# Kernel tuning notes

Measured on AMD Instinct MI355X. Metric: run time of the kernel, lower is better.

Reference implementation:

```python
import jax, jax.numpy as jnp
import numpy as np

B, G, NB, NC = 1024, 28, 2, 20
THR_CONF = 3.0
THR_NMS = 0.3
K = 4096            # fixed top-k detection slots (jit-friendly padding)
NEG = jnp.float32(-1e30)


def setup_inputs() -> dict:
    key = jax.random.key(0)
    k1, k2, k3 = jax.random.split(key, 3)
    return {
        "p_boxes": jax.random.normal(k1, (B, G, G, NB * 4), dtype=jnp.float32),
        "p_confs": jax.random.normal(k2, (B, G, G, NB), dtype=jnp.float32),
        "p_clses": jax.random.normal(k3, (B, G, G, NC), dtype=jnp.float32),
    }


def _decode_topk(p_boxes, p_confs, p_clses):
    # boxes: (B,G,G,NB,4) with (offx, offy, w, h) per box slot
    boxes = p_boxes.reshape(B, G, G, NB, 4)
    col = jnp.arange(G, dtype=jnp.float32)
    row = jnp.arange(G, dtype=jnp.float32)
    # offxy2xy: xy = (offxy + colrow) / num_grid  (dim1=row, dim2=col per torch.where order)
    cx = (boxes[..., 0] + col[None, None, :, None]) / G
    cy = (boxes[..., 1] + row[None, :, None, None]) / G
    w, h = boxes[..., 2], boxes[..., 3]
    # xywh2ltrb
    ltrb = jnp.stack([cx - w * 0.5, cy - h * 0.5, cx + w * 0.5, cy + h * 0.5], axis=-1)
    # label = argmax over classes + 1, shared by both box slots of a cell
    labels = jnp.argmax(p_clses, axis=-1) + 1                       # (B,G,G)
    labels = jnp.broadcast_to(labels[..., None], (B, G, G, NB))
    bids = jnp.broadcast_to(jnp.arange(B)[:, None, None, None], (B, G, G, NB))
    valid = p_confs > THR_CONF

    N = B * G * G * NB
    scores_masked = jnp.where(valid, p_confs, NEG).reshape(N)
    topv, topi = jax.lax.top_k(scores_masked, K)                    # sorted desc
    boxes_k = ltrb.reshape(N, 4)[topi]
    labels_k = labels.reshape(N)[topi]
    bids_k = bids.reshape(N)[topi]
    scores_k = p_confs.reshape(N)[topi]
    valid_k = topv > THR_CONF
    return bids_k, boxes_k, labels_k, scores_k, valid_k


def _iou_matrix(b):
    # b: (K,4) ltrb -> (K,K) pairwise IoU
    lt = jnp.maximum(b[:, None, :2], b[None, :, :2])
    rb = jnp.minimum(b[:, None, 2:], b[None, :, 2:])
    wh = jnp.clip(rb - lt, 0.0)
    inter = wh[..., 0] * wh[..., 1]
    area = jnp.clip(b[:, 2] - b[:, 0], 0.0) * jnp.clip(b[:, 3] - b[:, 1], 0.0)
    union = area[:, None] + area[None, :] - inter
    return inter / jnp.maximum(union, 1e-9)


def _nms(boxes, groups, valid):
    # per-(batch,label) NMS via group equality mask; boxes pre-sorted by score desc
    same = groups[:, None] == groups[None, :]
    suppress = same & (_iou_matrix(boxes) > THR_NMS)                # (K,K)
    idx = jnp.arange(K)

    def body(i, keep):
        sup = jnp.any(keep & suppress[:, i] & (idx < i))
        return keep.at[i].set(valid[i] & ~sup)

    return jax.lax.fori_loop(0, K, body, jnp.zeros((K,), dtype=bool))


def reference(p_boxes, p_confs, p_clses):
    bids, boxes, labels, scores, valid = _decode_topk(p_boxes, p_confs, p_clses)
    groups = bids * (NC + 1) + labels
    keep = _nms(boxes, groups, valid)
    # padded outputs of fixed size K; `keep` marks surviving detections
    return bids, boxes, labels, scores, keep
```

## Files before the change

### kernel.cpp

```cpp
#include <hip/hip_runtime.h>
#include <stdint.h>

#define B_    1024
#define G_    28
#define NB_   2
#define NC_   20
#define KK    4096
#define NTOT  (B_*G_*G_*NB_)
#define THRC  3.0f
#define THRN  0.3f
#define SORT_N 8192
#define NGRP  (B_*(NC_+1))
#define GCAP  8
#define RB    256
#define NRB2  (SORT_N/RB)
#define CPT   16

#define WS_CNT   0
#define WS_KEYS  256
#define WS_GLIST (WS_KEYS + SORT_N*8)
#define WS_GCNT  (WS_GLIST + KK*4)
#define WS_GMEM  (WS_GCNT + NGRP*4)

typedef unsigned long long u64;
typedef unsigned short u16;

__global__ void k_collect(const float4* __restrict__ conf4, u64* __restrict__ keys,
                          int* cnt, int* __restrict__ gcnt) {
    int t = blockIdx.x * blockDim.x + threadIdx.x;
    int lane = threadIdx.x & 63;
    if (t < NGRP) gcnt[t] = 0;
    float cc[CPT];
    #pragma unroll
    for (int q = 0; q < CPT / 4; ++q) {
        float4 v = conf4[t * (CPT / 4) + q];
        cc[q * 4 + 0] = v.x; cc[q * 4 + 1] = v.y;
        cc[q * 4 + 2] = v.z; cc[q * 4 + 3] = v.w;
    }
    int nh = 0;
    #pragma unroll
    for (int u = 0; u < CPT; ++u) nh += (cc[u] > THRC);
    u64 act = __ballot(nh > 0);
    if (act) {
        int incl = nh;
        #pragma unroll
        for (int off = 1; off < 64; off <<= 1) {
            int v = __shfl_up(incl, off);
            if (lane >= off) incl += v;
        }
        int tot = __shfl(incl, 63);
        int base = 0;
        if (lane == 0) base = atomicAdd(cnt, tot);
        base = __shfl(base, 0);
        int pos = base + incl - nh;
        int fb = t * CPT;
        #pragma unroll
        for (int u = 0; u < CPT; ++u) {
            if (cc[u] > THRC) {
                if (pos < SORT_N) {
                    unsigned b = __float_as_uint(cc[u]);
                    b = (b & 0x80000000u) ? ~b : (b | 0x80000000u);
                    keys[pos] = ((u64)b << 32) | (u64)(0xFFFFFFFFu - (unsigned)(fb + u));
                }
                pos++;
            }
        }
    }
}

struct Dec { int b; int lab; };
__device__ inline Dec decode_write(int slot, int idx, float score,
                                   const float* __restrict__ boxes,
                                   const float* __restrict__ clses,
                                   float* __restrict__ out) {
    int nb = idx & 1;
    int cell = idx >> 1;
    int gx = cell % G_;
    int t2 = cell / G_;
    int gy = t2 % G_;
    int b  = t2 / G_;
    float4 bv = *(const float4*)(boxes + (size_t)cell * (NB_ * 4) + nb * 4);
    float cx = (bv.x + (float)gx) / (float)G_;
    float cy = (bv.y + (float)gy) / (float)G_;
    float lf = cx - bv.z * 0.5f, tf = cy - bv.w * 0.5f;
    float rf = cx + bv.z * 0.5f, bf = cy + bv.w * 0.5f;
    const float4* cp4 = (const float4*)(clses + (size_t)cell * NC_);
    float best = -3.4e38f; int lab = 0;
    #pragma unroll
    for (int q = 0; q < 5; ++q) {
        float4 cv = cp4[q];
        float vv[4] = {cv.x, cv.y, cv.z, cv.w};
        #pragma unroll
        for (int u = 0; u < 4; ++u) {
            int ci = q * 4 + u;
            if (vv[u] > best) { best = vv[u]; lab = ci; }
        }
    }
    lab += 1;
    out[slot] = (float)b;
    *(float4*)(out + KK + 4*slot) = make_float4(lf, tf, rf, bf);
    out[5*KK + slot] = (float)lab;
    out[6*KK + slot] = score;
    out[7*KK + slot] = 0.0f;
    Dec d; d.b = b; d.lab = lab;
    return d;
}

__global__ void __launch_bounds__(RB) k_rankdec(const float* __restrict__ boxes,
                                                const float4* __restrict__ conf4,
                                                const float* __restrict__ conf,
                                                const float* __restrict__ clses,
                                                int* __restrict__ cnt,
                                                const u64* __restrict__ keys,
                                                float* __restrict__ out,
                                                int* __restrict__ glist,
                                                int* __restrict__ gcnt,
                                                u16* __restrict__ gmem) {
    int tid = threadIdx.x;
    int lane = tid & 63;
    int Vtot = min(cnt[0], SORT_N);
    int V = min(Vtot, KK);

    if (blockIdx.x == NRB2) {
        __shared__ int wsum[4];
        int M = KK - V;
        if (M <= 0) return;
        unsigned mask = 0;
        int base = tid * 32;
        #pragma unroll
        for (int q = 0; q < 8; ++q) {
            float4 cv = conf4[tid * 8 + q];
            mask |= (unsigned)(!(cv.x > THRC)) << (q * 4 + 0);
            mask |= (unsigned)(!(cv.y > THRC)) << (q * 4 + 1);
            mask |= (unsigned)(!(cv.z > THRC)) << (q * 4 + 2);
            mask |= (unsigned)(!(cv.w > THRC)) << (q * 4 + 3);
        }
        int c = __popc(mask);
        int incl = c;
        #pragma unroll
        for (int off = 1; off < 64; off <<= 1) {
            int v = __shfl_up(incl, off);
            if (lane >= off) incl += v;
        }
        int wid = tid >> 6;
        if (lane == 63) wsum[wid] = incl;
        __syncthreads();
        int wbase = 0;
        for (int w = 0; w < wid; ++w) wbase += wsum[w];
        int p = wbase + incl - c;
        unsigned m = mask;
        while (m) {
            int u = __builtin_ctz(m);
            if (p < M) {
                int idx = base + u;
                decode_write(V + p, idx, conf[idx], boxes, clses, out);
            }
            p++;
            m &= m - 1;
        }
        return;
    }

    __shared__ u64 sk[SORT_N];
    if (blockIdx.x * RB >= Vtot) return;
    const ulonglong2* keys2 = (const ulonglong2*)keys;
    for (int i = tid; i * 2 < Vtot; i += RB) {
        ulonglong2 kv = keys2[i];
        sk[2 * i]     = kv.x;
        sk[2 * i + 1] = kv.y;
    }
    __syncthreads();
    int t = blockIdx.x * RB + tid;
    if (t >= Vtot) return;
    u64 k0 = sk[t];
    int r = 0, j = 0;
    int lim = Vtot & ~7;
    for (; j < lim; j += 8) {
        r += (int)(sk[j+0] > k0) + (int)(sk[j+1] > k0)
           + (int)(sk[j+2] > k0) + (int)(sk[j+3] > k0)
           + (int)(sk[j+4] > k0) + (int)(sk[j+5] > k0)
           + (int)(sk[j+6] > k0) + (int)(sk[j+7] > k0);
    }
    for (; j < Vtot; ++j) r += (int)(sk[j] > k0);
    if (r >= KK) return;
    int idx = (int)(0xFFFFFFFFu - (unsigned)(k0 & 0xFFFFFFFFull));
    float score = __uint_as_float((unsigned)(k0 >> 32) ^ 0x80000000u);
    Dec d = decode_write(r, idx, score, boxes, clses, out);
    int g = d.b * (NC_ + 1) + d.lab;
    int pos = atomicAdd(&gcnt[g], 1);
    if (pos < GCAP) gmem[g * GCAP + pos] = (u16)r;
    if (pos == 0) {
        int gl = atomicAdd(&cnt[2], 1);
        glist[gl] = g;
    }
}

__global__ void k_nms(const int* __restrict__ cnt, const int* __restrict__ glist,
                      const int* __restrict__ gcnt, const u16* __restrict__ gmem,
                      float* __restrict__ out) {
    int t = blockIdx.x * blockDim.x + threadIdx.x;
    int ng = cnt[2];
    if (t >= ng) return;
    int g = glist[t];
    int m = min(gcnt[g], GCAP);
    u16 r[GCAP];
    for (int i = 0; i < m; ++i) r[i] = gmem[g * GCAP + i];
    for (int i = 1; i < m; ++i) {
        u16 v = r[i]; int j = i - 1;
        while (j >= 0 && r[j] > v) { r[j + 1] = r[j]; --j; }
        r[j + 1] = v;
    }
    if (m == 1) { out[7*KK + r[0]] = 1.0f; return; }
    float4 bx[GCAP]; float ar[GCAP];
    for (int i = 0; i < m; ++i) {
        bx[i] = *(const float4*)(out + KK + 4 * r[i]);
        ar[i] = fmaxf(bx[i].z - bx[i].x, 0.f) * fmaxf(bx[i].w - bx[i].y, 0.f);
    }
    unsigned keepm = 0;
    for (int i = 0; i < m; ++i) {
        bool sup = false;
        for (int j = 0; j < i; ++j) {
            if ((keepm >> j) & 1u) {
                float lx = fmaxf(bx[i].x, bx[j].x), ly = fmaxf(bx[i].y, bx[j].y);
                float rx = fminf(bx[i].z, bx[j].z), ry = fminf(bx[i].w, bx[j].w);
                float inter = fmaxf(rx - lx, 0.f) * fmaxf(ry - ly, 0.f);
                float uni = ar[i] + ar[j] - inter;
                if (inter / fmaxf(uni, 1e-9f) > THRN) sup = true;
            }
        }
        if (!sup) { keepm |= 1u << i; out[7*KK + r[i]] = 1.0f; }
    }
}

extern "C" void kernel_launch(void* const* d_in, const int* in_sizes, int n_in,
                              void* d_out, int out_size, void* d_ws, size_t ws_size,
                              hipStream_t stream) {
    const float* p_boxes = (const float*)d_in[0];
    const float* p_confs = (const float*)d_in[1];
    const float* p_clses = (const float*)d_in[2];
    float* out = (float*)d_out;
    char* ws = (char*)d_ws;

    int*  cnt   = (int*) (ws + WS_CNT);
    u64*  keys  = (u64*) (ws + WS_KEYS);
    int*  glist = (int*) (ws + WS_GLIST);
    int*  gcnt  = (int*) (ws + WS_GCNT);
    u16*  gmem  = (u16*) (ws + WS_GMEM);

    hipMemsetAsync(cnt, 0, 32, stream);
    k_collect<<<NTOT / CPT / 256, 256, 0, stream>>>((const float4*)p_confs, keys, cnt, gcnt);
    k_rankdec<<<NRB2 + 1, RB, 0, stream>>>(p_boxes, (const float4*)p_confs, p_confs,
                                           p_clses, cnt, keys, out, glist, gcnt, gmem);
    k_nms    <<<KK / 256, 256, 0, stream>>>(cnt, glist, gcnt, gmem, out);
}
```

Before: 58.60 us.

## Fold per-group NMS into rank kernel, building groups during collection

Group membership (batch, argmax label) is now computed in the collect kernel for every above-threshold score. Each group stores up to 8 sort keys, and the group counters are zeroed by a widened memset instead of inside the kernel. The separate NMS kernel and its group list are removed. Each ranked detection thread now sorts its group's keys, recomputes the boxes and runs the small greedy NMS redundantly to decide whether it survives, which saves one launch and one dependency. In exchange the per-thread work in the rank kernel grows, and groups now include candidates outside the top-K, which could change semantics when more than K detections pass the threshold.

```diff
diff --git a/kernel.cpp b/kernel.cpp
--- a/kernel.cpp
+++ b/kernel.cpp
@@ -17,19 +17,19 @@
 #define CPT   16
 
 #define WS_CNT   0
-#define WS_KEYS  256
-#define WS_GLIST (WS_KEYS + SORT_N*8)
-#define WS_GCNT  (WS_GLIST + KK*4)
-#define WS_GMEM  (WS_GCNT + NGRP*4)
+#define WS_GCNT  256
+#define WS_ZERO_BYTES (256 + NGRP*4)
+#define WS_KEYS  86272
+#define WS_GMEM  (WS_KEYS + SORT_N*8)
 
 typedef unsigned long long u64;
 typedef unsigned short u16;
 
-__global__ void k_collect(const float4* __restrict__ conf4, u64* __restrict__ keys,
-                          int* cnt, int* __restrict__ gcnt) {
+__global__ void k_collect(const float4* __restrict__ conf4, const float* __restrict__ clses,
+                          u64* __restrict__ keys, int* cnt,
+                          int* __restrict__ gcnt, u64* __restrict__ gmem) {
     int t = blockIdx.x * blockDim.x + threadIdx.x;
     int lane = threadIdx.x & 63;
-    if (t < NGRP) gcnt[t] = 0;
     float cc[CPT];
     #pragma unroll
     for (int q = 0; q < CPT / 4; ++q) {
@@ -57,15 +57,43 @@
         #pragma unroll
         for (int u = 0; u < CPT; ++u) {
             if (cc[u] > THRC) {
-                if (pos < SORT_N) {
-                    unsigned b = __float_as_uint(cc[u]);
-                    b = (b & 0x80000000u) ? ~b : (b | 0x80000000u);
-                    keys[pos] = ((u64)b << 32) | (u64)(0xFFFFFFFFu - (unsigned)(fb + u));
+                int idx = fb + u;
+                unsigned b = __float_as_uint(cc[u]);
+                b = (b & 0x80000000u) ? ~b : (b | 0x80000000u);
+                u64 key = ((u64)b << 32) | (u64)(0xFFFFFFFFu - (unsigned)idx);
+                if (pos < SORT_N) keys[pos] = key;
+                pos++;
+                int cell = idx >> 1;
+                const float4* cp4 = (const float4*)(clses + (size_t)cell * NC_);
+                float best = -3.4e38f; int lab = 0;
+                #pragma unroll
+                for (int q = 0; q < 5; ++q) {
+                    float4 cv = cp4[q];
+                    float vv[4] = {cv.x, cv.y, cv.z, cv.w};
+                    #pragma unroll
+                    for (int w = 0; w < 4; ++w) {
+                        int ci = q * 4 + w;
+                        if (vv[w] > best) { best = vv[w]; lab = ci; }
+                    }
                 }
-                pos++;
+                int g = (cell / (G_ * G_)) * (NC_ + 1) + (lab + 1);
+                int p2 = atomicAdd(&gcnt[g], 1);
+                if (p2 < GCAP) gmem[(size_t)g * GCAP + p2] = key;
             }
         }
     }
+}
+
+__device__ inline float4 box_of(int idx, const float* __restrict__ boxes) {
+    int nb = idx & 1;
+    int cell = idx >> 1;
+    int gx = cell % G_;
+    int gy = (cell / G_) % G_;
+    float4 bv = *(const float4*)(boxes + (size_t)cell * (NB_ * 4) + nb * 4);
+    float cx = (bv.x + (float)gx) / (float)G_;
+    float cy = (bv.y + (float)gy) / (float)G_;
+    return make_float4(cx - bv.z * 0.5f, cy - bv.w * 0.5f,
+                       cx + bv.z * 0.5f, cy + bv.w * 0.5f);
 }
 
 struct Dec { int b; int lab; };
@@ -73,17 +101,9 @@
                                    const float* __restrict__ boxes,
                                    const float* __restrict__ clses,
                                    float* __restrict__ out) {
-    int nb = idx & 1;
     int cell = idx >> 1;
-    int gx = cell % G_;
-    int t2 = cell / G_;
-    int gy = t2 % G_;
-    int b  = t2 / G_;
-    float4 bv = *(const float4*)(boxes + (size_t)cell * (NB_ * 4) + nb * 4);
-    float cx = (bv.x + (float)gx) / (float)G_;
-    float cy = (bv.y + (float)gy) / (float)G_;
-    float lf = cx - bv.z * 0.5f, tf = cy - bv.w * 0.5f;
-    float rf = cx + bv.z * 0.5f, bf = cy + bv.w * 0.5f;
+    int b = cell / (G_ * G_);
+    float4 lt = box_of(idx, boxes);
     const float4* cp4 = (const float4*)(clses + (size_t)cell * NC_);
     float best = -3.4e38f; int lab = 0;
     #pragma unroll
@@ -98,7 +118,7 @@
     }
     lab += 1;
     out[slot] = (float)b;
-    *(float4*)(out + KK + 4*slot) = make_float4(lf, tf, rf, bf);
+    *(float4*)(out + KK + 4*slot) = lt;
     out[5*KK + slot] = (float)lab;
     out[6*KK + slot] = score;
     out[7*KK + slot] = 0.0f;
@@ -110,12 +130,11 @@
                                                 const float4* __restrict__ conf4,
                                                 const float* __restrict__ conf,
                                                 const float* __restrict__ clses,
-                                                int* __restrict__ cnt,
+                                                const int* __restrict__ cnt,
                                                 const u64* __restrict__ keys,
                                                 float* __restrict__ out,
-                                                int* __restrict__ glist,
-                                                int* __restrict__ gcnt,
-                                                u16* __restrict__ gmem) {
+                                                const int* __restrict__ gcnt,
+                                                const u64* __restrict__ gmem) {
     int tid = threadIdx.x;
     int lane = tid & 63;
     int Vtot = min(cnt[0], SORT_N);
@@ -186,50 +205,45 @@
     int idx = (int)(0xFFFFFFFFu - (unsigned)(k0 & 0xFFFFFFFFull));
     float score = __uint_as_float((unsigned)(k0 >> 32) ^ 0x80000000u);
     Dec d = decode_write(r, idx, score, boxes, clses, out);
+
     int g = d.b * (NC_ + 1) + d.lab;
-    int pos = atomicAdd(&gcnt[g], 1);
-    if (pos < GCAP) gmem[g * GCAP + pos] = (u16)r;
-    if (pos == 0) {
-        int gl = atomicAdd(&cnt[2], 1);
-        glist[gl] = g;
-    }
-}
-
-__global__ void k_nms(const int* __restrict__ cnt, const int* __restrict__ glist,
-                      const int* __restrict__ gcnt, const u16* __restrict__ gmem,
-                      float* __restrict__ out) {
-    int t = blockIdx.x * blockDim.x + threadIdx.x;
-    int ng = cnt[2];
-    if (t >= ng) return;
-    int g = glist[t];
     int m = min(gcnt[g], GCAP);
-    u16 r[GCAP];
-    for (int i = 0; i < m; ++i) r[i] = gmem[g * GCAP + i];
+    u64 mem[GCAP];
+    for (int i = 0; i < m; ++i) mem[i] = gmem[(size_t)g * GCAP + i];
     for (int i = 1; i < m; ++i) {
-        u16 v = r[i]; int j = i - 1;
-        while (j >= 0 && r[j] > v) { r[j + 1] = r[j]; --j; }
-        r[j + 1] = v;
-    }
-    if (m == 1) { out[7*KK + r[0]] = 1.0f; return; }
-    float4 bx[GCAP]; float ar[GCAP];
-    for (int i = 0; i < m; ++i) {
-        bx[i] = *(const float4*)(out + KK + 4 * r[i]);
-        ar[i] = fmaxf(bx[i].z - bx[i].x, 0.f) * fmaxf(bx[i].w - bx[i].y, 0.f);
-    }
-    unsigned keepm = 0;
-    for (int i = 0; i < m; ++i) {
-        bool sup = false;
-        for (int j = 0; j < i; ++j) {
-            if ((keepm >> j) & 1u) {
-                float lx = fmaxf(bx[i].x, bx[j].x), ly = fmaxf(bx[i].y, bx[j].y);
-                float rx = fminf(bx[i].z, bx[j].z), ry = fminf(bx[i].w, bx[j].w);
-                float inter = fmaxf(rx - lx, 0.f) * fmaxf(ry - ly, 0.f);
-                float uni = ar[i] + ar[j] - inter;
-                if (inter / fmaxf(uni, 1e-9f) > THRN) sup = true;
+        u64 v = mem[i]; int q = i - 1;
+        while (q >= 0 && mem[q] < v) { mem[q + 1] = mem[q]; --q; }
+        mem[q + 1] = v;
+    }
+    bool survive;
+    if (m <= 1) {
+        survive = true;
+    } else {
+        int own = 0;
+        float4 bx[GCAP]; float ar[GCAP];
+        for (int i = 0; i < m; ++i) {
+            if (mem[i] == k0) own = i;
+            int mi = (int)(0xFFFFFFFFu - (unsigned)(mem[i] & 0xFFFFFFFFull));
+            bx[i] = box_of(mi, boxes);
+            ar[i] = fmaxf(bx[i].z - bx[i].x, 0.f) * fmaxf(bx[i].w - bx[i].y, 0.f);
+        }
+        unsigned keepm = 0;
+        for (int i = 0; i < m; ++i) {
+            bool sup = false;
+            for (int q = 0; q < i; ++q) {
+                if ((keepm >> q) & 1u) {
+                    float lx = fmaxf(bx[i].x, bx[q].x), ly = fmaxf(bx[i].y, bx[q].y);
+                    float rx = fminf(bx[i].z, bx[q].z), ry = fminf(bx[i].w, bx[q].w);
+                    float inter = fmaxf(rx - lx, 0.f) * fmaxf(ry - ly, 0.f);
+                    float uni = ar[i] + ar[q] - inter;
+                    if (inter / fmaxf(uni, 1e-9f) > THRN) sup = true;
+                }
             }
-        }
-        if (!sup) { keepm |= 1u << i; out[7*KK + r[i]] = 1.0f; }
-    }
+            if (!sup) keepm |= 1u << i;
+        }
+        survive = (keepm >> own) & 1u;
+    }
+    if (survive) out[7*KK + r] = 1.0f;
 }
 
 extern "C" void kernel_launch(void* const* d_in, const int* in_sizes, int n_in,
@@ -242,14 +256,13 @@
     char* ws = (char*)d_ws;
 
     int*  cnt   = (int*) (ws + WS_CNT);
+    int*  gcnt  = (int*) (ws + WS_GCNT);
     u64*  keys  = (u64*) (ws + WS_KEYS);
-    int*  glist = (int*) (ws + WS_GLIST);
-    int*  gcnt  = (int*) (ws + WS_GCNT);
-    u16*  gmem  = (u16*) (ws + WS_GMEM);
-
-    hipMemsetAsync(cnt, 0, 32, stream);
-    k_collect<<<NTOT / CPT / 256, 256, 0, stream>>>((const float4*)p_confs, keys, cnt, gcnt);
+    u64*  gmem  = (u64*) (ws + WS_GMEM);
+
+    hipMemsetAsync(ws, 0, WS_ZERO_BYTES, stream);
+    k_collect<<<NTOT / CPT / 256, 256, 0, stream>>>((const float4*)p_confs, p_clses,
+                                                    keys, cnt, gcnt, gmem);
     k_rankdec<<<NRB2 + 1, RB, 0, stream>>>(p_boxes, (const float4*)p_confs, p_confs,
-                                           p_clses, cnt, keys, out, glist, gcnt, gmem);
-    k_nms    <<<KK / 256, 256, 0, stream>>>(cnt, glist, gcnt, gmem, out);
-}
+                                           p_clses, cnt, keys, out, gcnt, gmem);
+}
```

After: 58.99 us. No clear change (+0.7%).
